# Kernel tuning notes

Hardware: AMD Instinct MI355X
Metric: run time of the kernel (lower is better)

## Reference

```python
import jax, jax.numpy as jnp
import numpy as np

NUM_GRAPHS = 32      # equal-sized graphs; batch = node_id // (N // NUM_GRAPHS)
RATIO = 0.5
NEG_SLOPE = 0.2
BN_EPS = 1e-5


def setup_inputs() -> dict:
    key = jax.random.key(0)
    k0, k1, k2, k3, k4 = jax.random.split(key, 5)
    N, Cin, Cout, E = 65536, 256, 128, 1048576
    x = jax.random.normal(k0, (N, Cin), dtype=jnp.float32)
    # edges with no self loops (remove_self_loops is then a no-op)
    src = jax.random.randint(k1, (E,), 0, N, dtype=jnp.int32)
    off = jax.random.randint(k2, (E,), 1, N, dtype=jnp.int32)
    dst = (src + off) % N
    edge_index = jnp.stack([src, dst])  # [2, E], row0=source j, row1=target i
    batch = jnp.repeat(jnp.arange(NUM_GRAPHS, dtype=jnp.int32), N // NUM_GRAPHS)
    # glorot init for weight and att
    s_w = float(np.sqrt(6.0 / (Cin + Cout)))
    W = jax.random.uniform(k3, (Cin, Cout), jnp.float32, -s_w, s_w)
    s_a = float(np.sqrt(6.0 / (1 + 2 * Cout)))
    att = jax.random.uniform(k4, (2 * Cout,), jnp.float32, -s_a, s_a)
    bn_gamma = jnp.ones((Cout,), jnp.float32)
    bn_beta = jnp.zeros((Cout,), jnp.float32)
    return {"x": x, "W": W, "att": att, "bn_gamma": bn_gamma, "bn_beta": bn_beta,
            "edge_index": edge_index, "batch": batch, "bn": 1}


def reference(x, W, att, bn_gamma, bn_beta, edge_index, batch, bn):
    N = x.shape[0]
    C = W.shape[1]
    loops = jnp.arange(N, dtype=edge_index.dtype)
    src = jnp.concatenate([edge_index[0], loops])  # source j
    dst = jnp.concatenate([edge_index[1], loops])  # target i
    xw = x @ W  # [N, C]
    # alpha_e = (cat[x_i, x_j] * att).sum(-1) = x_i.att[:C] + x_j.att[C:]
    a_i = xw @ att[:C]
    a_j = xw @ att[C:]
    alpha = a_i[dst] + a_j[src]
    alpha = jnp.where(alpha >= 0, alpha, NEG_SLOPE * alpha)  # leaky_relu
    # edge softmax grouped by target node (edge_index_i)
    seg_max = jax.ops.segment_max(alpha, dst, num_segments=N)
    seg_max = jnp.where(jnp.isfinite(seg_max), seg_max, 0.0)
    ex = jnp.exp(alpha - seg_max[dst])
    denom = jax.ops.segment_sum(ex, dst, num_segments=N)  # >0 (self loops)
    alpha = ex / denom[dst]
    # per-source-node attention mass
    alpha_sum = jax.ops.segment_sum(alpha, src, num_segments=N)
    # per-graph top-k node selection (equal graph sizes -> static shapes)
    n = N // NUM_GRAPHS
    k = int(n * RATIO)
    scores = alpha_sum.reshape(NUM_GRAPHS, n)
    _, idx = jax.lax.top_k(scores, k)                       # [B, k]
    perm = (idx + jnp.arange(NUM_GRAPHS)[:, None] * n).reshape(-1)  # global node ids
    topk_batch = jnp.repeat(jnp.arange(NUM_GRAPHS, dtype=batch.dtype), k)
    # delete_node: keep only edges whose endpoints both survive
    keep = jnp.zeros((N,), bool).at[perm].set(True)
    emask = keep[src] & keep[dst]
    scale = jnp.where(emask, alpha, 0.0)
    msg = xw[src] * scale[:, None]                          # [E+N, C] gather
    out = jax.ops.segment_sum(msg, dst, num_segments=N)     # scatter-add aggr
    out_final = out[perm]                                   # [B*k, C]
    if bn:
        mu = out_final.mean(axis=0)
        var = out_final.var(axis=0)
        out_final = (out_final - mu) * jax.lax.rsqrt(var + BN_EPS) * bn_gamma + bn_beta
    return (out_final, perm, topk_batch)
```

## Files before the change

kernel.cpp:

```cpp
#include <hip/hip_runtime.h>
#include <math.h>

#define CIN 256
#define COUT 128
#define NGRAPH 32
#define NCHUNK 256

__global__ __launch_bounds__(256) void gemm_csr(const float* __restrict__ x,
                                                const float* __restrict__ W,
                                                float* __restrict__ xw,
                                                const int* __restrict__ esrc,
                                                const int* __restrict__ edst,
                                                int* __restrict__ deg,
                                                unsigned short* __restrict__ csr_j,
                                                int* __restrict__ outdeg,
                                                unsigned short* __restrict__ csr_i,
                                                int E, int M, int nGemm) {
    __shared__ float xs[32][68];
    __shared__ float ws[32][132];
    if ((int)blockIdx.x < nGemm) {
        int t = threadIdx.x;
        int bm0 = blockIdx.x * 64;
        int tx = t & 15;
        int ty = t >> 4;
        float acc[4][8];
#pragma unroll
        for (int i = 0; i < 4; ++i)
#pragma unroll
            for (int j = 0; j < 8; ++j) acc[i][j] = 0.0f;

        for (int kc = 0; kc < CIN / 32; ++kc) {
            int k0 = kc * 32;
            {
                int ml = t >> 2, kq = (t & 3) * 8;
                const float* sp = x + (size_t)(bm0 + ml) * CIN + k0 + kq;
                float4 v0 = ((const float4*)sp)[0];
                float4 v1 = ((const float4*)sp)[1];
                xs[kq + 0][ml] = v0.x;  xs[kq + 1][ml] = v0.y;
                xs[kq + 2][ml] = v0.z;  xs[kq + 3][ml] = v0.w;
                xs[kq + 4][ml] = v1.x;  xs[kq + 5][ml] = v1.y;
                xs[kq + 6][ml] = v1.z;  xs[kq + 7][ml] = v1.w;
            }
            {
                int kl = t >> 3, n0 = (t & 7) * 16;
                const float* sp = W + (size_t)(k0 + kl) * COUT + n0;
#pragma unroll
                for (int w4 = 0; w4 < 4; ++w4)
                    *(float4*)&ws[kl][n0 + 4 * w4] = *(const float4*)(sp + 4 * w4);
            }
            __syncthreads();
#pragma unroll 4
            for (int kk = 0; kk < 32; ++kk) {
                float aa[4], bb[8];
                *(float4*)&aa[0] = *(float4*)&xs[kk][tx * 4];
                *(float4*)&bb[0] = *(float4*)&ws[kk][ty * 8];
                *(float4*)&bb[4] = *(float4*)&ws[kk][ty * 8 + 4];
#pragma unroll
                for (int i = 0; i < 4; ++i)
#pragma unroll
                    for (int j = 0; j < 8; ++j) acc[i][j] += aa[i] * bb[j];
            }
            __syncthreads();
        }
#pragma unroll
        for (int i = 0; i < 4; ++i) {
            float* dp = xw + (size_t)(bm0 + tx * 4 + i) * COUT + ty * 8;
            float4 s0 = {acc[i][0], acc[i][1], acc[i][2], acc[i][3]};
            float4 s1 = {acc[i][4], acc[i][5], acc[i][6], acc[i][7]};
            *(float4*)dp = s0;
            *(float4*)(dp + 4) = s1;
        }
        return;
    }
    int bid = blockIdx.x - nGemm;
    int k = bid & 7;
    int r = bid >> 3;
    int lo = k << 13, hi = lo + 8192;
    int pairs = M >> 1;
    int chunkP = (pairs + NCHUNK - 1) / NCHUNK;
    int p0 = r * chunkP;
    int p1 = p0 + chunkP; if (p1 > pairs) p1 = pairs;
    for (int p = p0 + threadIdx.x; p < p1; p += 256) {
        int e0 = p * 2;
        int i0, j0, i1, j1;
        if (e0 < E) {
            int2 js = *(const int2*)(esrc + e0);
            int2 is = *(const int2*)(edst + e0);
            j0 = js.x; j1 = js.y; i0 = is.x; i1 = is.y;
        } else {
            i0 = j0 = e0 - E; i1 = j1 = e0 + 1 - E;
        }
        if (i0 >= lo && i0 < hi) {
            int s0 = atomicAdd(&deg[i0], 1);
            if (s0 < 64) csr_j[(i0 << 6) + s0] = (unsigned short)j0;
        }
        if (i1 >= lo && i1 < hi) {
            int s1 = atomicAdd(&deg[i1], 1);
            if (s1 < 64) csr_j[(i1 << 6) + s1] = (unsigned short)j1;
        }
        if (j0 >= lo && j0 < hi) {
            int s0 = atomicAdd(&outdeg[j0], 1);
            if (s0 < 64) csr_i[(j0 << 6) + s0] = (unsigned short)i0;
        }
        if (j1 >= lo && j1 < hi) {
            int s1 = atomicAdd(&outdeg[j1], 1);
            if (s1 < 64) csr_i[(j1 << 6) + s1] = (unsigned short)i1;
        }
    }
}

__global__ __launch_bounds__(256) void aij32_kernel(const float* __restrict__ xw,
                                                    const float* __restrict__ att,
                                                    float* __restrict__ a_i,
                                                    float* __restrict__ a_j) {
    __shared__ float sa[2 * COUT];
    int t = threadIdx.x;
    sa[t] = att[t];
    __syncthreads();
    int n = blockIdx.x * 256 + t;
    const float* row = xw + (size_t)n * COUT;
    float ai = 0.0f, aj = 0.0f;
#pragma unroll 8
    for (int c = 0; c < COUT; c += 4) {
        float4 f = *(const float4*)(row + c);
        ai += f.x * sa[c];     aj += f.x * sa[COUT + c];
        ai += f.y * sa[c + 1]; aj += f.y * sa[COUT + c + 1];
        ai += f.z * sa[c + 2]; aj += f.z * sa[COUT + c + 2];
        ai += f.w * sa[c + 3]; aj += f.w * sa[COUT + c + 3];
    }
    a_i[n] = ai;
    a_j[n] = aj;
}

__global__ __launch_bounds__(256) void node_softmax(const int* __restrict__ deg,
                                                    const unsigned short* __restrict__ csr_j,
                                                    const float* __restrict__ a_i,
                                                    const float* __restrict__ a_j,
                                                    float* __restrict__ mbuf,
                                                    float* __restrict__ dbuf) {
    int t = threadIdx.x;
    int g = t & 15;
    int node = blockIdx.x * 16 + (t >> 4);
    int d = deg[node];
    if (d > 64) d = 64;
    float ai = a_i[node];
    int base = node << 6;
    ushort4 jraw = *(const ushort4*)(csr_j + base + 4 * g);
    unsigned short js[4] = {jraw.x, jraw.y, jraw.z, jraw.w};
    float l[4];
    int jj[4];
    float lm = -INFINITY;
#pragma unroll
    for (int q = 0; q < 4; ++q) {
        int p = 4 * g + q;
        if (p < d) {
            int j = (int)js[q];
            float lv = ai + a_j[j];
            lv = (lv >= 0.0f) ? lv : 0.2f * lv;
            jj[q] = j; l[q] = lv;
            lm = fmaxf(lm, lv);
        } else {
            jj[q] = -1;
        }
    }
#pragma unroll
    for (int mk = 1; mk < 16; mk <<= 1)
        lm = fmaxf(lm, __shfl_xor(lm, mk, 16));
    double ds = 0.0;
#pragma unroll
    for (int q = 0; q < 4; ++q) {
        if (jj[q] >= 0) {
            float ex = expf(l[q] - lm);
            ds += (double)ex;
        }
    }
#pragma unroll
    for (int mk = 1; mk < 16; mk <<= 1)
        ds += __shfl_xor(ds, mk, 16);
    float df = (float)ds;
    if (g == 0) { mbuf[node] = lm; dbuf[node] = df; }
}

__global__ __launch_bounds__(256) void node_asum(const int* __restrict__ outdeg,
                                                 const unsigned short* __restrict__ csr_i,
                                                 const float* __restrict__ a_i,
                                                 const float* __restrict__ a_j,
                                                 const float* __restrict__ mbuf,
                                                 const float* __restrict__ dbuf,
                                                 double* __restrict__ asum) {
    int t = threadIdx.x;
    int g = t & 15;
    int node = blockIdx.x * 16 + (t >> 4);
    int d = outdeg[node];
    if (d > 64) d = 64;
    float aj = a_j[node];
    int base = node << 6;
    ushort4 iraw = *(const ushort4*)(csr_i + base + 4 * g);
    unsigned short is[4] = {iraw.x, iraw.y, iraw.z, iraw.w};
    double ds = 0.0;
#pragma unroll
    for (int q = 0; q < 4; ++q) {
        int p = 4 * g + q;
        if (p < d) {
            int ii = (int)is[q];
            float l = a_i[ii] + aj;
            l = (l >= 0.0f) ? l : 0.2f * l;
            float al = expf(l - mbuf[ii]) / dbuf[ii];
            ds += (double)al;
        }
    }
#pragma unroll
    for (int mk = 1; mk < 16; mk <<= 1)
        ds += __shfl_xor(ds, mk, 16);
    if (g == 0) asum[node] = ds;
}

__global__ __launch_bounds__(256) void rank_kernel(const double* __restrict__ asum,
                                                   int* __restrict__ rank,
                                                   float* __restrict__ out,
                                                   int* __restrict__ perm_int,
                                                   double* __restrict__ bnacc,
                                                   int perG, int kSel,
                                                   int permOff, int tbOff) {
    __shared__ float sc[2048];
    int bpg = perG >> 8;
    int g = blockIdx.x / bpg;
    int sub = blockIdx.x - g * bpg;
    int t = threadIdx.x;
    if (blockIdx.x == 0) bnacc[t] = 0.0;
    for (int q = t; q < perG; q += 256)
        sc[q] = (float)asum[g * perG + q];
    __syncthreads();
    int m = sub * 256 + t;
    float s = sc[m];
    int r = 0;
#pragma unroll 4
    for (int q4 = 0; q4 < 2048; q4 += 4) {
        float4 f = *(const float4*)&sc[q4];
        r += (int)((f.x > s) || (f.x == s && (q4 + 0) < m));
        r += (int)((f.y > s) || (f.y == s && (q4 + 1) < m));
        r += (int)((f.z > s) || (f.z == s && (q4 + 2) < m));
        r += (int)((f.w > s) || (f.w == s && (q4 + 3) < m));
    }
    int node = g * perG + m;
    if (r < kSel) {
        int pos = g * kSel + r;
        rank[node] = pos;
        perm_int[pos] = node;
        out[permOff + pos] = (float)node;
        out[tbOff + pos] = (float)g;
    } else {
        rank[node] = -1;
    }
}

__global__ __launch_bounds__(256) void aggr_kernel(const int* __restrict__ perm_int,
                                                   const int* __restrict__ deg,
                                                   const unsigned short* __restrict__ csr_j,
                                                   const int* __restrict__ rank,
                                                   const float* __restrict__ a_i,
                                                   const float* __restrict__ a_j,
                                                   const float* __restrict__ mbuf,
                                                   const float* __restrict__ dbuf,
                                                   const float* __restrict__ xw,
                                                   float* __restrict__ outf, int R) {
    int wid = (int)((blockIdx.x * 256u + threadIdx.x) >> 6);
    int lane = threadIdx.x & 63;
    if (wid >= R) return;
    int node = perm_int[wid];
    int d = deg[node];
    if (d > 64) d = 64;
    float ai = a_i[node];
    float m = mbuf[node];
    float df = dbuf[node];
    int base = node << 6;
    int jv = 0, kv = 0;
    float alv = 0.0f;
    if (lane < d) {
        jv = (int)csr_j[base + lane];
        if (rank[jv] >= 0) {
            float l = ai + a_j[jv];
            l = (l >= 0.0f) ? l : 0.2f * l;
            alv = expf(l - m) / df;
            kv = 1;
        }
    }
    float2 acc = {0.0f, 0.0f};
    for (int p = 0; p < d; ++p) {
        int keep = __shfl(kv, p, 64);
        if (!keep) continue;
        int j = __shfl(jv, p, 64);
        float al = __shfl(alv, p, 64);
        float2 xv = *(const float2*)(xw + (size_t)j * COUT + lane * 2);
        acc.x += xv.x * al;
        acc.y += xv.y * al;
    }
    *(float2*)(outf + (size_t)wid * COUT + lane * 2) = acc;
}

__global__ __launch_bounds__(256) void bn_stats(const float* __restrict__ outf,
                                                double* __restrict__ acc, int R) {
    int t = threadIdx.x;
    int c = t & 127;
    int r0 = blockIdx.x * 2 + (t >> 7);
    double s = 0.0, s2 = 0.0;
    for (int r = r0; r < R; r += 512) {
        double v = (double)outf[(size_t)r * COUT + c];
        s += v; s2 += v * v;
    }
    atomicAdd(&acc[c], s);
    atomicAdd(&acc[128 + c], s2);
}

__global__ void bn_apply(float* __restrict__ outf, const double* __restrict__ acc,
                         const float* __restrict__ gamma, const float* __restrict__ beta,
                         const int* __restrict__ bnflag, int R) {
    int idx = blockIdx.x * blockDim.x + threadIdx.x;
    if (idx >= R * COUT) return;
    if (*bnflag == 0) return;
    int c = idx & 127;
    double invR = 1.0 / (double)R;
    double mu = acc[c] * invR;
    double var = acc[128 + c] * invR - mu * mu;
    double inv = 1.0 / sqrt(var + 1e-5);
    outf[idx] = (float)(((double)outf[idx] - mu) * inv * (double)gamma[c] + (double)beta[c]);
}

extern "C" void kernel_launch(void* const* d_in, const int* in_sizes, int n_in,
                              void* d_out, int out_size, void* d_ws, size_t ws_size,
                              hipStream_t stream) {
    const float* x     = (const float*)d_in[0];
    const float* W     = (const float*)d_in[1];
    const float* att   = (const float*)d_in[2];
    const float* gamma = (const float*)d_in[3];
    const float* beta  = (const float*)d_in[4];
    const int*   eidx  = (const int*)d_in[5];
    const int*   bnfl  = (const int*)d_in[7];

    const int N = in_sizes[0] / CIN;
    const int E = in_sizes[5] / 2;
    const int M = E + N;
    const int perG = N / NGRAPH;
    const int kSel = perG / 2;
    const int R = NGRAPH * kSel;
    const int permOff = R * COUT;
    const int tbOff = permOff + R;

    const int* esrc = eidx;
    const int* edst = eidx + E;

    char* w = (char*)d_ws;
    float*  xw     = (float*)w;             w += (size_t)N * COUT * 4;
    float*  a_i    = (float*)w;             w += (size_t)N * 4;
    float*  a_j    = (float*)w;             w += (size_t)N * 4;
    int*    deg    = (int*)w;               w += (size_t)N * 4;
    int*    outdeg = (int*)w;               w += (size_t)N * 4;
    double* asum   = (double*)w;            w += (size_t)N * 8;
    float*  mbuf   = (float*)w;             w += (size_t)N * 4;
    float*  dbuf   = (float*)w;             w += (size_t)N * 4;
    unsigned short* csr_j = (unsigned short*)w; w += (size_t)N * 64 * 2;
    unsigned short* csr_i = (unsigned short*)w; w += (size_t)N * 64 * 2;
    int*    rank   = (int*)w;               w += (size_t)N * 4;
    int*    perm_int = (int*)w;             w += (size_t)R * 4;
    double* bnacc  = (double*)w;            w += 256 * 8;

    float* out = (float*)d_out;

    hipMemsetAsync(deg, 0, (size_t)N * (4 + 4), stream);

    const int nGemm = N / 64;
    gemm_csr<<<nGemm + NCHUNK * 8, 256, 0, stream>>>(x, W, xw, esrc, edst,
                                                     deg, csr_j, outdeg, csr_i,
                                                     E, M, nGemm);

    aij32_kernel<<<N / 256, 256, 0, stream>>>(xw, att, a_i, a_j);

    node_softmax<<<N / 16, 256, 0, stream>>>(deg, csr_j, a_i, a_j, mbuf, dbuf);

    node_asum<<<N / 16, 256, 0, stream>>>(outdeg, csr_i, a_i, a_j, mbuf, dbuf, asum);

    rank_kernel<<<NGRAPH * (perG >> 8), 256, 0, stream>>>(asum, rank, out, perm_int,
                                                          bnacc, perG, kSel, permOff, tbOff);

    aggr_kernel<<<(R * 64 + 255) / 256, 256, 0, stream>>>(perm_int, deg, csr_j, rank,
                                                          a_i, a_j, mbuf, dbuf, xw, out, R);

    bn_stats<<<256, 256, 0, stream>>>(out, bnacc, R);
    bn_apply<<<(R * COUT + 255) / 256, 256, 0, stream>>>(out, bnacc, gamma, beta, bnfl, R);
}
```

Before: 388.5 us.

## Move outgoing-edge CSR build from GEMM kernel into softmax kernel

The reverse CSR construction (outdeg/csr_i by source node) is split out of the combined GEMM+CSR kernel and attached as extra blocks to the node softmax kernel. The GEMM kernel now only builds the incoming CSR, which shortens its scatter phase. The reverse scatter then runs alongside the softmax work, which is otherwise latency-bound. The cost is that the edge arrays are read a second time, and the softmax launch is now larger and mixes two kinds of work.

New measurement: 395.3 us. Within noise of the previous version (+1.8%).

```diff
diff --git a/kernel.cpp b/kernel.cpp
--- a/kernel.cpp
+++ b/kernel.cpp
@@ -13,8 +13,6 @@
                                                 const int* __restrict__ edst,
                                                 int* __restrict__ deg,
                                                 unsigned short* __restrict__ csr_j,
-                                                int* __restrict__ outdeg,
-                                                unsigned short* __restrict__ csr_i,
                                                 int E, int M, int nGemm) {
     __shared__ float xs[32][68];
     __shared__ float ws[32][132];
@@ -97,14 +95,6 @@
         if (i1 >= lo && i1 < hi) {
             int s1 = atomicAdd(&deg[i1], 1);
             if (s1 < 64) csr_j[(i1 << 6) + s1] = (unsigned short)j1;
-        }
-        if (j0 >= lo && j0 < hi) {
-            int s0 = atomicAdd(&outdeg[j0], 1);
-            if (s0 < 64) csr_i[(j0 << 6) + s0] = (unsigned short)i0;
-        }
-        if (j1 >= lo && j1 < hi) {
-            int s1 = atomicAdd(&outdeg[j1], 1);
-            if (s1 < 64) csr_i[(j1 << 6) + s1] = (unsigned short)i1;
         }
     }
 }
@@ -132,53 +122,84 @@
     a_j[n] = aj;
 }
 
-__global__ __launch_bounds__(256) void node_softmax(const int* __restrict__ deg,
-                                                    const unsigned short* __restrict__ csr_j,
-                                                    const float* __restrict__ a_i,
-                                                    const float* __restrict__ a_j,
-                                                    float* __restrict__ mbuf,
-                                                    float* __restrict__ dbuf) {
-    int t = threadIdx.x;
-    int g = t & 15;
-    int node = blockIdx.x * 16 + (t >> 4);
-    int d = deg[node];
-    if (d > 64) d = 64;
-    float ai = a_i[node];
-    int base = node << 6;
-    ushort4 jraw = *(const ushort4*)(csr_j + base + 4 * g);
-    unsigned short js[4] = {jraw.x, jraw.y, jraw.z, jraw.w};
-    float l[4];
-    int jj[4];
-    float lm = -INFINITY;
-#pragma unroll
-    for (int q = 0; q < 4; ++q) {
-        int p = 4 * g + q;
-        if (p < d) {
-            int j = (int)js[q];
-            float lv = ai + a_j[j];
-            lv = (lv >= 0.0f) ? lv : 0.2f * lv;
-            jj[q] = j; l[q] = lv;
-            lm = fmaxf(lm, lv);
+__global__ __launch_bounds__(256) void softmax_scatter(
+    const int* __restrict__ deg, const unsigned short* __restrict__ csr_j,
+    const float* __restrict__ a_i, const float* __restrict__ a_j,
+    float* __restrict__ mbuf, float* __restrict__ dbuf,
+    const int* __restrict__ esrc, const int* __restrict__ edst,
+    int* __restrict__ outdeg, unsigned short* __restrict__ csr_i,
+    int E, int M, int nSm) {
+    if ((int)blockIdx.x < nSm) {
+        int t = threadIdx.x;
+        int g = t & 15;
+        int node = blockIdx.x * 16 + (t >> 4);
+        int d = deg[node];
+        if (d > 64) d = 64;
+        float ai = a_i[node];
+        int base = node << 6;
+        ushort4 jraw = *(const ushort4*)(csr_j + base + 4 * g);
+        unsigned short js[4] = {jraw.x, jraw.y, jraw.z, jraw.w};
+        float l[4];
+        int jj[4];
+        float lm = -INFINITY;
+#pragma unroll
+        for (int q = 0; q < 4; ++q) {
+            int p = 4 * g + q;
+            if (p < d) {
+                int j = (int)js[q];
+                float lv = ai + a_j[j];
+                lv = (lv >= 0.0f) ? lv : 0.2f * lv;
+                jj[q] = j; l[q] = lv;
+                lm = fmaxf(lm, lv);
+            } else {
+                jj[q] = -1;
+            }
+        }
+#pragma unroll
+        for (int mk = 1; mk < 16; mk <<= 1)
+            lm = fmaxf(lm, __shfl_xor(lm, mk, 16));
+        double ds = 0.0;
+#pragma unroll
+        for (int q = 0; q < 4; ++q) {
+            if (jj[q] >= 0) {
+                float ex = expf(l[q] - lm);
+                ds += (double)ex;
+            }
+        }
+#pragma unroll
+        for (int mk = 1; mk < 16; mk <<= 1)
+            ds += __shfl_xor(ds, mk, 16);
+        float df = (float)ds;
+        if (g == 0) { mbuf[node] = lm; dbuf[node] = df; }
+        return;
+    }
+    int bid = blockIdx.x - nSm;
+    int k = bid & 7;
+    int r = bid >> 3;
+    int lo = k << 13, hi = lo + 8192;
+    int pairs = M >> 1;
+    int chunkP = (pairs + NCHUNK - 1) / NCHUNK;
+    int p0 = r * chunkP;
+    int p1 = p0 + chunkP; if (p1 > pairs) p1 = pairs;
+    for (int p = p0 + threadIdx.x; p < p1; p += 256) {
+        int e0 = p * 2;
+        int i0, j0, i1, j1;
+        if (e0 < E) {
+            int2 js = *(const int2*)(esrc + e0);
+            int2 is = *(const int2*)(edst + e0);
+            j0 = js.x; j1 = js.y; i0 = is.x; i1 = is.y;
         } else {
-            jj[q] = -1;
-        }
-    }
-#pragma unroll
-    for (int mk = 1; mk < 16; mk <<= 1)
-        lm = fmaxf(lm, __shfl_xor(lm, mk, 16));
-    double ds = 0.0;
-#pragma unroll
-    for (int q = 0; q < 4; ++q) {
-        if (jj[q] >= 0) {
-            float ex = expf(l[q] - lm);
-            ds += (double)ex;
-        }
-    }
-#pragma unroll
-    for (int mk = 1; mk < 16; mk <<= 1)
-        ds += __shfl_xor(ds, mk, 16);
-    float df = (float)ds;
-    if (g == 0) { mbuf[node] = lm; dbuf[node] = df; }
+            i0 = j0 = e0 - E; i1 = j1 = e0 + 1 - E;
+        }
+        if (j0 >= lo && j0 < hi) {
+            int s0 = atomicAdd(&outdeg[j0], 1);
+            if (s0 < 64) csr_i[(j0 << 6) + s0] = (unsigned short)i0;
+        }
+        if (j1 >= lo && j1 < hi) {
+            int s1 = atomicAdd(&outdeg[j1], 1);
+            if (s1 < 64) csr_i[(j1 << 6) + s1] = (unsigned short)i1;
+        }
+    }
 }
 
 __global__ __launch_bounds__(256) void node_asum(const int* __restrict__ outdeg,
@@ -370,12 +391,14 @@
 
     const int nGemm = N / 64;
     gemm_csr<<<nGemm + NCHUNK * 8, 256, 0, stream>>>(x, W, xw, esrc, edst,
-                                                     deg, csr_j, outdeg, csr_i,
-                                                     E, M, nGemm);
+                                                     deg, csr_j, E, M, nGemm);
 
     aij32_kernel<<<N / 256, 256, 0, stream>>>(xw, att, a_i, a_j);
 
-    node_softmax<<<N / 16, 256, 0, stream>>>(deg, csr_j, a_i, a_j, mbuf, dbuf);
+    const int nSm = N / 16;
+    softmax_scatter<<<nSm + NCHUNK * 8, 256, 0, stream>>>(deg, csr_j, a_i, a_j,
+                                                          mbuf, dbuf, esrc, edst,
+                                                          outdeg, csr_i, E, M, nSm);
 
     node_asum<<<N / 16, 256, 0, stream>>>(outdeg, csr_i, a_i, a_j, mbuf, dbuf, asum);
 
```
